# Kernel tuning notes

Hardware: AMD Instinct MI355X
Metric: run time of the kernel (lower is better)

Reference implementation:

```python
import jax, jax.numpy as jnp
import numpy as np

Nx, Nu, Ny, Np, H = 2, 1, 2, 8, 32
Nz = Np * (Nx + Nu)  # 24
B, T = 4096, 256
F, V, Delta = 0.1, 1.0, 1.0  # ps.squeeze(), volume, sample time
ymean = jnp.array([0.5, 0.5], jnp.float32)
ystd = jnp.array([0.3, 0.2], jnp.float32)
umean = jnp.array([1.0], jnp.float32)
ustd = jnp.array([0.5], jnp.float32)


def fnn(x, params):
    # dense layers: tanh hidden, linear output
    for W, b in params[:-1]:
        x = jnp.tanh(x @ W + b)
    W, b = params[-1]
    return x @ W + b


def fxzu(x, z, u, p1, p2, p3):
    # dCa/dt = F*(Caf-Ca)/V - r1 ; dCb/dt = -F*Cb/V + r1 - 3*r2 + r3
    Castd, Cbstd = ystd[0:1], ystd[1:2]
    r1 = fnn(x[:, 0:1], p1) * Castd
    r2 = fnn(x[:, 1:2], p2) * Cbstd
    r3 = fnn(z, p3) * Cbstd
    xs = x * ystd + ymean
    us = u * ustd + umean
    Ca, Cb, Caf = xs[:, 0:1], xs[:, 1:2], us[:, 0:1]
    dCa = F * (Caf - Ca) / V - r1
    dCb = -F * Cb / V + r1 - 3.0 * r2 + r3
    return jnp.concatenate([dCa, dCb], axis=-1) / ystd


def interp(yseq):
    # (B,(Np+1)*Nx) -> (B, Np*Nx): midpoints of consecutive Nx-blocks
    b = yseq.shape[0]
    y = yseq.reshape(b, Np + 1, Nx)
    return (0.5 * (y[:, :-1] + y[:, 1:])).reshape(b, Np * Nx)


def run(useq, xz0, p1, p2, p3):
    def step(xz, u):
        x, z = xz[:, :Nx], xz[:, Nx:]
        xpseq, upseq = z[:, :Np * Nx], z[:, Np * Nx:]
        k1 = fxzu(x, z, u, p1, p2, p3)
        z23 = jnp.concatenate([interp(jnp.concatenate([xpseq, x], -1)), upseq], -1)
        k2 = fxzu(x + Delta * k1 / 2, z23, u, p1, p2, p3)
        k3 = fxzu(x + Delta * k2 / 2, z23, u, p1, p2, p3)
        z4 = jnp.concatenate([xpseq[:, Nx:], x, upseq], -1)
        k4 = fxzu(x + Delta * k3, z4, u, p1, p2, p3)
        xplus = x + (Delta / 6.0) * (k1 + 2 * k2 + 2 * k3 + k4)
        zplus = jnp.concatenate([xpseq[:, Nx:], x, upseq[:, Nu:], u], -1)
        return jnp.concatenate([xplus, zplus], -1), x  # output is pre-update x
    _, ys = jax.lax.scan(step, xz0, jnp.swapaxes(useq, 0, 1))
    return jnp.swapaxes(ys, 0, 1)  # (B, T, Ny)


def setup_inputs() -> dict:
    key = jax.random.key(0)
    ks = jax.random.split(key, 12)
    inp = {
        'useq': jax.random.normal(ks[0], (B, T, Nu), jnp.float32),
        'xz0': jax.random.normal(ks[1], (B, Nx + Nz), jnp.float32),
    }
    dims = {'r1': [1, H, H, 1], 'r2': [1, H, H, 1], 'r3': [Nz, H, H, 1]}
    i = 2
    for name, ds in dims.items():
        for l, (din, dout) in enumerate(zip(ds[:-1], ds[1:])):
            inp[f'{name}W{l}'] = jax.random.normal(ks[i], (din, dout), jnp.float32) / np.sqrt(din).astype(np.float32)
            inp[f'{name}b{l}'] = jnp.zeros((dout,), jnp.float32)
            i += 1
    return inp


def reference(useq, xz0, r1W0, r1b0, r1W1, r1b1, r1W2, r1b2,
              r2W0, r2b0, r2W1, r2b1, r2W2, r2b2,
              r3W0, r3b0, r3W1, r3b1, r3W2, r3b2):
    p1 = [(r1W0, r1b0), (r1W1, r1b1), (r1W2, r1b2)]
    p2 = [(r2W0, r2b0), (r2W1, r2b1), (r2W2, r2b2)]
    p3 = [(r3W0, r3b0), (r3W1, r3b1), (r3W2, r3b2)]
    return run(useq, xz0, p1, p2, p3)
```

## Files before the change

kernel.cpp:

```cpp
#include <hip/hip_runtime.h>

#define DEVINL static __device__ __forceinline__
#define LDSBAR() asm volatile("s_waitcnt lgkmcnt(0)" ::: "memory")

DEVINL float tanh_fast(float x) {
  float e = __expf(2.0f * x);
  return 1.0f - 2.0f * __builtin_amdgcn_rcpf(e + 1.0f);
}

template <int CTRL>
DEVINL float dpp_add(float v) {
  int t = __builtin_amdgcn_update_dpp(0, __float_as_int(v), CTRL, 0xF, 0xF, true);
  return v + __int_as_float(t);
}
DEVINL float rsum32(float v) {
  v = dpp_add<0xB1>(v);
  v = dpp_add<0x4E>(v);
  v = dpp_add<0x141>(v);
  v = dpp_add<0x140>(v);
  v += __int_as_float(__builtin_amdgcn_ds_swizzle(__float_as_int(v), 0x401F));
  return v;
}

DEVINL float dot4(float4 v, const float* w) {
  return fmaf(v.x, w[0], fmaf(v.y, w[1], fmaf(v.z, w[2], v.w * w[3])));
}
DEVINL float dot32(const float4* hp, const float* W, float bias) {
  float a0 = bias, a1 = 0.f, a2 = 0.f, a3 = 0.f;
#pragma unroll
  for (int q = 0; q < 8; q += 4) {
    float4 h0 = hp[q], h1 = hp[q + 1], h2 = hp[q + 2], h3 = hp[q + 3];
    a0 = fmaf(h0.x, W[4 * q + 0], a0);  a0 = fmaf(h0.y, W[4 * q + 1], a0);
    a0 = fmaf(h0.z, W[4 * q + 2], a0);  a0 = fmaf(h0.w, W[4 * q + 3], a0);
    a1 = fmaf(h1.x, W[4 * q + 4], a1);  a1 = fmaf(h1.y, W[4 * q + 5], a1);
    a1 = fmaf(h1.z, W[4 * q + 6], a1);  a1 = fmaf(h1.w, W[4 * q + 7], a1);
    a2 = fmaf(h2.x, W[4 * q + 8], a2);  a2 = fmaf(h2.y, W[4 * q + 9], a2);
    a2 = fmaf(h2.z, W[4 * q + 10], a2); a2 = fmaf(h2.w, W[4 * q + 11], a2);
    a3 = fmaf(h3.x, W[4 * q + 12], a3); a3 = fmaf(h3.y, W[4 * q + 13], a3);
    a3 = fmaf(h3.z, W[4 * q + 14], a3); a3 = fmaf(h3.w, W[4 * q + 15], a3);
  }
  return (a0 + a1) + (a2 + a3);
}

constexpr int TSTEPS = 256;

__global__ __launch_bounds__(64, 2) void reac_kernel(
    const float* __restrict__ useq,
    const float* __restrict__ xz0,
    const float* __restrict__ r1W0, const float* __restrict__ r1b0,
    const float* __restrict__ r1W1, const float* __restrict__ r1b1,
    const float* __restrict__ r1W2, const float* __restrict__ r1b2,
    const float* __restrict__ r2W0, const float* __restrict__ r2b0,
    const float* __restrict__ r2W1, const float* __restrict__ r2b1,
    const float* __restrict__ r2W2, const float* __restrict__ r2b2,
    const float* __restrict__ r3W0, const float* __restrict__ r3b0,
    const float* __restrict__ r3W1, const float* __restrict__ r3b1,
    const float* __restrict__ r3W2, const float* __restrict__ r3b2,
    float2* __restrict__ out)
{
  const int lane = threadIdx.x;
  const int bl = lane >> 5;
  const int j  = lane & 31;
  const int b  = blockIdx.x * 2 + bl;

  float w0A = r1W0[j], b0A = r1b0[j];
  float w0B = r2W0[j], b0B = r2b0[j];
  float b1A = r1b1[j], b1B = r2b1[j];
  float w2A = r1W2[j], w2B = r2W2[j];
  float b2A = r1b2[0], b2B = r2b2[0];
  float b0C = r3b0[j], b1C = r3b1[j];
  float w2C = r3W2[j], b2C = r3b2[0];

  float W1A[32], W1B[32], W1C[32], W0C[24];
#pragma unroll
  for (int k = 0; k < 32; ++k) {
    W1A[k] = r1W1[k * 32 + j];
    W1B[k] = r2W1[k * 32 + j];
    W1C[k] = r3W1[k * 32 + j];
  }
#pragma unroll
  for (int k = 0; k < 24; ++k) W0C[k] = r3W0[k * 32 + j];

  __shared__ __align__(16) float zs[2][24];
  __shared__ __align__(16) float zb[2][16];
  __shared__ __align__(16) float hA[2][32];
  __shared__ __align__(16) float hB[2][32];
  __shared__ __align__(16) float hR3[2][3][32];

  float x0 = xz0[b * 26 + 0];
  float x1 = xz0[b * 26 + 1];
  if (j < 24) zs[bl][j] = xz0[b * 26 + 2 + j];
  LDSBAR();

  auto eval_r12 = [&](float s0, float s1, float& ra, float& rb) {
    float h1a = tanh_fast(fmaf(s0, w0A, b0A));
    float h1b = tanh_fast(fmaf(s1, w0B, b0B));
    hA[bl][j] = h1a;
    hB[bl][j] = h1b;
    LDSBAR();
    float aA = dot32((const float4*)&hA[bl][0], W1A, b1A);
    float aB = dot32((const float4*)&hB[bl][0], W1B, b1B);
    ra = (rsum32(tanh_fast(aA) * w2A) + b2A) * 0.3f;
    rb = (rsum32(tanh_fast(aB) * w2B) + b2B) * 0.2f;
  };

  auto mixk = [&](float sx0, float sx1, float Caf, float ra, float rb, float rc,
                  float& kx, float& ky) {
    float Ca = fmaf(sx0, 0.3f, 0.5f);
    float Cb = fmaf(sx1, 0.2f, 0.5f);
    float dCa = 0.1f * (Caf - Ca) - ra;
    float dCb = fmaf(-0.1f, Cb, ra - 3.0f * rb + rc);
    kx = dCa * (1.0f / 0.3f);
    ky = dCb * (1.0f / 0.2f);
  };

  float u = useq[b * TSTEPS];

  for (int t = 0; t < TSTEPS; ++t) {
    int tn = (t < TSTEPS - 1) ? (t + 1) : t;
    float u_nxt = useq[b * TSTEPS + tn];
    float Caf = fmaf(u, 0.5f, 1.0f);

    if (j == 0) out[b * TSTEPS + t] = make_float2(x0, x1);

    if (j < 16) {
      zb[bl][j] = (j < 14) ? zs[bl][j + 2] : ((j == 14) ? x0 : x1);
    }
    LDSBAR();

    const float4* zsp = (const float4*)&zs[bl][0];
    const float4* zbp = (const float4*)&zb[bl][0];
    float4 za0 = zsp[0], za1 = zsp[1], za2 = zsp[2], za3 = zsp[3];
    float4 zu0 = zsp[4], zu1 = zsp[5];
    float4 q0 = zbp[0], q1 = zbp[1], q2 = zbp[2], q3 = zbp[3];
    float accS = (dot4(za0, W0C) + dot4(za1, W0C + 4)) +
                 (dot4(za2, W0C + 8) + dot4(za3, W0C + 12));
    float accB = (dot4(q0, W0C) + dot4(q1, W0C + 4)) +
                 (dot4(q2, W0C + 8) + dot4(q3, W0C + 12));
    float accU = dot4(zu0, W0C + 16) + dot4(zu1, W0C + 20) + b0C;
    float a1v = accS + accU;
    float a4v = accB + accU;
    float a23v = fmaf(0.5f, accS + accB, accU);
    hR3[bl][0][j] = tanh_fast(a1v);
    hR3[bl][1][j] = tanh_fast(a23v);
    hR3[bl][2][j] = tanh_fast(a4v);
    LDSBAR();
    float o1 = dot32((const float4*)&hR3[bl][0][0], W1C, b1C);
    float o23 = dot32((const float4*)&hR3[bl][1][0], W1C, b1C);
    float o4 = dot32((const float4*)&hR3[bl][2][0], W1C, b1C);
    float rc1 = (rsum32(tanh_fast(o1) * w2C) + b2C) * 0.2f;
    float rc23 = (rsum32(tanh_fast(o23) * w2C) + b2C) * 0.2f;
    float rc4 = (rsum32(tanh_fast(o4) * w2C) + b2C) * 0.2f;

    float ra, rb, kx1, ky1, kx2, ky2, kx3, ky3, kx4, ky4;
    eval_r12(x0, x1, ra, rb);
    mixk(x0, x1, Caf, ra, rb, rc1, kx1, ky1);

    float sx = fmaf(kx1, 0.5f, x0), sy = fmaf(ky1, 0.5f, x1);
    eval_r12(sx, sy, ra, rb);
    mixk(sx, sy, Caf, ra, rb, rc23, kx2, ky2);

    sx = fmaf(kx2, 0.5f, x0); sy = fmaf(ky2, 0.5f, x1);
    eval_r12(sx, sy, ra, rb);
    mixk(sx, sy, Caf, ra, rb, rc23, kx3, ky3);

    sx = x0 + kx3; sy = x1 + ky3;
    eval_r12(sx, sy, ra, rb);
    mixk(sx, sy, Caf, ra, rb, rc4, kx4, ky4);

    float znew = 0.0f;
    if (j < 16) znew = zb[bl][j];
    else if (j < 23) znew = zs[bl][j + 1];
    else if (j == 23) znew = u;
    LDSBAR();
    if (j < 24) zs[bl][j] = znew;
    x0 += (kx1 + 2.0f * (kx2 + kx3) + kx4) * (1.0f / 6.0f);
    x1 += (ky1 + 2.0f * (ky2 + ky3) + ky4) * (1.0f / 6.0f);
    u = u_nxt;
    LDSBAR();
  }
}

extern "C" void kernel_launch(void* const* d_in, const int* in_sizes, int n_in,
                              void* d_out, int out_size, void* d_ws, size_t ws_size,
                              hipStream_t stream) {
  const float* p[20];
  for (int i = 0; i < 20; ++i) p[i] = (const float*)d_in[i];
  reac_kernel<<<dim3(2048), dim3(64), 0, stream>>>(
      p[0], p[1], p[2], p[3], p[4], p[5], p[6], p[7], p[8], p[9], p[10],
      p[11], p[12], p[13], p[14], p[15], p[16], p[17], p[18], p[19],
      (float2*)d_out);
}
```

Measured before the change: 943.9 us.

## Map one batch row per wavefront, splitting r1/r2 and r3 work across half-waves

```diff
diff --git a/kernel.cpp b/kernel.cpp
--- a/kernel.cpp
+++ b/kernel.cpp
@@ -25,26 +25,38 @@
 DEVINL float dot4(float4 v, const float* w) {
   return fmaf(v.x, w[0], fmaf(v.y, w[1], fmaf(v.z, w[2], v.w * w[3])));
 }
-DEVINL float dot32(const float4* hp, const float* W, float bias) {
+DEVINL float dot32(const float* hrow, const float* W, float bias) {
+  const float4* hp = (const float4*)hrow;
   float a0 = bias, a1 = 0.f, a2 = 0.f, a3 = 0.f;
 #pragma unroll
-  for (int q = 0; q < 8; q += 4) {
-    float4 h0 = hp[q], h1 = hp[q + 1], h2 = hp[q + 2], h3 = hp[q + 3];
-    a0 = fmaf(h0.x, W[4 * q + 0], a0);  a0 = fmaf(h0.y, W[4 * q + 1], a0);
-    a0 = fmaf(h0.z, W[4 * q + 2], a0);  a0 = fmaf(h0.w, W[4 * q + 3], a0);
-    a1 = fmaf(h1.x, W[4 * q + 4], a1);  a1 = fmaf(h1.y, W[4 * q + 5], a1);
-    a1 = fmaf(h1.z, W[4 * q + 6], a1);  a1 = fmaf(h1.w, W[4 * q + 7], a1);
-    a2 = fmaf(h2.x, W[4 * q + 8], a2);  a2 = fmaf(h2.y, W[4 * q + 9], a2);
-    a2 = fmaf(h2.z, W[4 * q + 10], a2); a2 = fmaf(h2.w, W[4 * q + 11], a2);
-    a3 = fmaf(h3.x, W[4 * q + 12], a3); a3 = fmaf(h3.y, W[4 * q + 13], a3);
-    a3 = fmaf(h3.z, W[4 * q + 14], a3); a3 = fmaf(h3.w, W[4 * q + 15], a3);
+  for (int q = 0; q < 8; q += 2) {
+    float4 x = hp[q], y = hp[q + 1];
+    a0 = fmaf(x.x, W[4 * q + 0], a0); a1 = fmaf(x.y, W[4 * q + 1], a1);
+    a2 = fmaf(x.z, W[4 * q + 2], a2); a3 = fmaf(x.w, W[4 * q + 3], a3);
+    a0 = fmaf(y.x, W[4 * q + 4], a0); a1 = fmaf(y.y, W[4 * q + 5], a1);
+    a2 = fmaf(y.z, W[4 * q + 6], a2); a3 = fmaf(y.w, W[4 * q + 7], a3);
   }
+  return (a0 + a1) + (a2 + a3);
+}
+DEVINL float pdot16(const float* hrow, const float* W) {
+  const float4* hp = (const float4*)hrow;
+  float a0 = 0.f, a1 = 0.f, a2 = 0.f, a3 = 0.f;
+  float4 x = hp[0], y = hp[1];
+  a0 = fmaf(x.x, W[0], a0);  a1 = fmaf(x.y, W[1], a1);
+  a2 = fmaf(x.z, W[2], a2);  a3 = fmaf(x.w, W[3], a3);
+  a0 = fmaf(y.x, W[4], a0);  a1 = fmaf(y.y, W[5], a1);
+  a2 = fmaf(y.z, W[6], a2);  a3 = fmaf(y.w, W[7], a3);
+  x = hp[2]; y = hp[3];
+  a0 = fmaf(x.x, W[8], a0);  a1 = fmaf(x.y, W[9], a1);
+  a2 = fmaf(x.z, W[10], a2); a3 = fmaf(x.w, W[11], a3);
+  a0 = fmaf(y.x, W[12], a0); a1 = fmaf(y.y, W[13], a1);
+  a2 = fmaf(y.z, W[14], a2); a3 = fmaf(y.w, W[15], a3);
   return (a0 + a1) + (a2 + a3);
 }
 
 constexpr int TSTEPS = 256;
 
-__global__ __launch_bounds__(64, 2) void reac_kernel(
+__global__ __launch_bounds__(64, 4) void reac_kernel(
     const float* __restrict__ useq,
     const float* __restrict__ xz0,
     const float* __restrict__ r1W0, const float* __restrict__ r1b0,
@@ -59,55 +71,56 @@
     float2* __restrict__ out)
 {
   const int lane = threadIdx.x;
-  const int bl = lane >> 5;
-  const int j  = lane & 31;
-  const int b  = blockIdx.x * 2 + bl;
+  const int j = lane & 31;
+  const bool hi = lane >= 32;
+  const int b = blockIdx.x;
 
-  float w0A = r1W0[j], b0A = r1b0[j];
-  float w0B = r2W0[j], b0B = r2b0[j];
-  float b1A = r1b1[j], b1B = r2b1[j];
-  float w2A = r1W2[j], w2B = r2W2[j];
-  float b2A = r1b2[0], b2B = r2b2[0];
-  float b0C = r3b0[j], b1C = r3b1[j];
-  float w2C = r3W2[j], b2C = r3b2[0];
+  const float* W0p = hi ? r2W0 : r1W0;
+  const float* B0p = hi ? r2b0 : r1b0;
+  const float* W1p = hi ? r2W1 : r1W1;
+  const float* B1p = hi ? r2b1 : r1b1;
+  const float* W2p = hi ? r2W2 : r1W2;
+  const float* B2p = hi ? r2b2 : r1b2;
+  float w0 = W0p[j], b0 = B0p[j], b1 = B1p[j], w2 = W2p[j], b2 = B2p[0];
+  float sc = hi ? 0.2f : 0.3f;
 
-  float W1A[32], W1B[32], W1C[32], W0C[24];
+  float W1[32];
 #pragma unroll
-  for (int k = 0; k < 32; ++k) {
-    W1A[k] = r1W1[k * 32 + j];
-    W1B[k] = r2W1[k * 32 + j];
-    W1C[k] = r3W1[k * 32 + j];
-  }
+  for (int k = 0; k < 32; ++k) W1[k] = W1p[k * 32 + j];
+
+  float W0C[24];
 #pragma unroll
-  for (int k = 0; k < 24; ++k) W0C[k] = r3W0[k * 32 + j];
+  for (int m = 0; m < 24; ++m) W0C[m] = r3W0[m * 32 + j];
+  const int kbase = hi ? 16 : 0;
+  float W1C[16];
+#pragma unroll
+  for (int k = 0; k < 16; ++k) W1C[k] = r3W1[(kbase + k) * 32 + j];
+  float b0C = r3b0[j], b1C = r3b1[j], w2C = r3W2[j], b2C = r3b2[0];
 
-  __shared__ __align__(16) float zs[2][24];
-  __shared__ __align__(16) float zb[2][16];
-  __shared__ __align__(16) float hA[2][32];
-  __shared__ __align__(16) float hB[2][32];
-  __shared__ __align__(16) float hR3[2][3][32];
+  __shared__ __align__(16) float zs[24];
+  __shared__ __align__(16) float zb[16];
+  __shared__ __align__(16) float h12[2][32];
+  __shared__ __align__(16) float hR3[3][32];
 
   float x0 = xz0[b * 26 + 0];
   float x1 = xz0[b * 26 + 1];
-  if (j < 24) zs[bl][j] = xz0[b * 26 + 2 + j];
+  if (!hi && j < 24) zs[j] = xz0[b * 26 + 2 + j];
   LDSBAR();
 
-  auto eval_r12 = [&](float s0, float s1, float& ra, float& rb) {
-    float h1a = tanh_fast(fmaf(s0, w0A, b0A));
-    float h1b = tanh_fast(fmaf(s1, w0B, b0B));
-    hA[bl][j] = h1a;
-    hB[bl][j] = h1b;
+  auto stage = [&](float sxv, float syv, float rc, float Caf,
+                   float& kx, float& ky) {
+    float s = hi ? syv : sxv;
+    float h = tanh_fast(fmaf(s, w0, b0));
     LDSBAR();
-    float aA = dot32((const float4*)&hA[bl][0], W1A, b1A);
-    float aB = dot32((const float4*)&hB[bl][0], W1B, b1B);
-    ra = (rsum32(tanh_fast(aA) * w2A) + b2A) * 0.3f;
-    rb = (rsum32(tanh_fast(aB) * w2B) + b2B) * 0.2f;
-  };
-
-  auto mixk = [&](float sx0, float sx1, float Caf, float ra, float rb, float rc,
-                  float& kx, float& ky) {
-    float Ca = fmaf(sx0, 0.3f, 0.5f);
-    float Cb = fmaf(sx1, 0.2f, 0.5f);
+    h12[hi][j] = h;
+    LDSBAR();
+    float a = dot32(&h12[hi][0], W1, b1);
+    float r = (rsum32(tanh_fast(a) * w2) + b2) * sc;
+    float rp = __shfl_xor(r, 32);
+    float ra = hi ? rp : r;
+    float rb = hi ? r : rp;
+    float Ca = fmaf(sxv, 0.3f, 0.5f);
+    float Cb = fmaf(syv, 0.2f, 0.5f);
     float dCa = 0.1f * (Caf - Ca) - ra;
     float dCb = fmaf(-0.1f, Cb, ra - 3.0f * rb + rc);
     kx = dCa * (1.0f / 0.3f);
@@ -121,59 +134,51 @@
     float u_nxt = useq[b * TSTEPS + tn];
     float Caf = fmaf(u, 0.5f, 1.0f);
 
-    if (j == 0) out[b * TSTEPS + t] = make_float2(x0, x1);
+    if (lane == 0) out[b * TSTEPS + t] = make_float2(x0, x1);
 
-    if (j < 16) {
-      zb[bl][j] = (j < 14) ? zs[bl][j + 2] : ((j == 14) ? x0 : x1);
+    if (!hi && j < 16) {
+      zb[j] = (j < 14) ? zs[j + 2] : ((j == 14) ? x0 : x1);
     }
     LDSBAR();
 
-    const float4* zsp = (const float4*)&zs[bl][0];
-    const float4* zbp = (const float4*)&zb[bl][0];
-    float4 za0 = zsp[0], za1 = zsp[1], za2 = zsp[2], za3 = zsp[3];
-    float4 zu0 = zsp[4], zu1 = zsp[5];
-    float4 q0 = zbp[0], q1 = zbp[1], q2 = zbp[2], q3 = zbp[3];
-    float accS = (dot4(za0, W0C) + dot4(za1, W0C + 4)) +
-                 (dot4(za2, W0C + 8) + dot4(za3, W0C + 12));
-    float accB = (dot4(q0, W0C) + dot4(q1, W0C + 4)) +
-                 (dot4(q2, W0C + 8) + dot4(q3, W0C + 12));
-    float accU = dot4(zu0, W0C + 16) + dot4(zu1, W0C + 20) + b0C;
-    float a1v = accS + accU;
-    float a4v = accB + accU;
-    float a23v = fmaf(0.5f, accS + accB, accU);
-    hR3[bl][0][j] = tanh_fast(a1v);
-    hR3[bl][1][j] = tanh_fast(a23v);
-    hR3[bl][2][j] = tanh_fast(a4v);
+    const float4* zp = (const float4*)(hi ? &zb[0] : &zs[0]);
+    float4 z0 = zp[0], z1 = zp[1], z2 = zp[2], z3 = zp[3];
+    const float4* up = (const float4*)&zs[16];
+    float4 u0 = up[0], u1 = up[1];
+    float A = b0C +
+        ((dot4(z0, W0C) + dot4(z1, W0C + 4)) +
+         (dot4(z2, W0C + 8) + dot4(z3, W0C + 12))) +
+        (dot4(u0, W0C + 16) + dot4(u1, W0C + 20));
+    float Ap = __shfl_xor(A, 32);
+    float tA = tanh_fast(A);
+    if (!hi) {
+      hR3[0][j] = tA;
+      hR3[1][j] = tanh_fast(0.5f * (A + Ap));
+    } else {
+      hR3[2][j] = tA;
+    }
     LDSBAR();
-    float o1 = dot32((const float4*)&hR3[bl][0][0], W1C, b1C);
-    float o23 = dot32((const float4*)&hR3[bl][1][0], W1C, b1C);
-    float o4 = dot32((const float4*)&hR3[bl][2][0], W1C, b1C);
-    float rc1 = (rsum32(tanh_fast(o1) * w2C) + b2C) * 0.2f;
-    float rc23 = (rsum32(tanh_fast(o23) * w2C) + b2C) * 0.2f;
-    float rc4 = (rsum32(tanh_fast(o4) * w2C) + b2C) * 0.2f;
+    float p0 = pdot16(&hR3[0][kbase], W1C);
+    float p1 = pdot16(&hR3[1][kbase], W1C);
+    float p2 = pdot16(&hR3[2][kbase], W1C);
+    float o0 = p0 + __shfl_xor(p0, 32) + b1C;
+    float o1 = p1 + __shfl_xor(p1, 32) + b1C;
+    float o2 = p2 + __shfl_xor(p2, 32) + b1C;
+    float rc1  = (rsum32(tanh_fast(o0) * w2C) + b2C) * 0.2f;
+    float rc23 = (rsum32(tanh_fast(o1) * w2C) + b2C) * 0.2f;
+    float rc4  = (rsum32(tanh_fast(o2) * w2C) + b2C) * 0.2f;
 
-    float ra, rb, kx1, ky1, kx2, ky2, kx3, ky3, kx4, ky4;
-    eval_r12(x0, x1, ra, rb);
-    mixk(x0, x1, Caf, ra, rb, rc1, kx1, ky1);
-
-    float sx = fmaf(kx1, 0.5f, x0), sy = fmaf(ky1, 0.5f, x1);
-    eval_r12(sx, sy, ra, rb);
-    mixk(sx, sy, Caf, ra, rb, rc23, kx2, ky2);
-
-    sx = fmaf(kx2, 0.5f, x0); sy = fmaf(ky2, 0.5f, x1);
-    eval_r12(sx, sy, ra, rb);
-    mixk(sx, sy, Caf, ra, rb, rc23, kx3, ky3);
-
-    sx = x0 + kx3; sy = x1 + ky3;
-    eval_r12(sx, sy, ra, rb);
-    mixk(sx, sy, Caf, ra, rb, rc4, kx4, ky4);
+    float kx1, ky1, kx2, ky2, kx3, ky3, kx4, ky4;
+    stage(x0, x1, rc1, Caf, kx1, ky1);
+    stage(fmaf(kx1, 0.5f, x0), fmaf(ky1, 0.5f, x1), rc23, Caf, kx2, ky2);
+    stage(fmaf(kx2, 0.5f, x0), fmaf(ky2, 0.5f, x1), rc23, Caf, kx3, ky3);
+    stage(x0 + kx3, x1 + ky3, rc4, Caf, kx4, ky4);
 
     float znew = 0.0f;
-    if (j < 16) znew = zb[bl][j];
-    else if (j < 23) znew = zs[bl][j + 1];
-    else if (j == 23) znew = u;
+    bool updz = (!hi) && (j < 24);
+    if (updz) znew = (j < 16) ? zb[j] : ((j < 23) ? zs[j + 1] : u);
     LDSBAR();
-    if (j < 24) zs[bl][j] = znew;
+    if (updz) zs[j] = znew;
     x0 += (kx1 + 2.0f * (kx2 + kx3) + kx4) * (1.0f / 6.0f);
     x1 += (ky1 + 2.0f * (ky2 + ky3) + ky4) * (1.0f / 6.0f);
     u = u_nxt;
@@ -186,7 +191,7 @@
                               hipStream_t stream) {
   const float* p[20];
   for (int i = 0; i < 20; ++i) p[i] = (const float*)d_in[i];
-  reac_kernel<<<dim3(2048), dim3(64), 0, stream>>>(
+  reac_kernel<<<dim3(4096), dim3(64), 0, stream>>>(
       p[0], p[1], p[2], p[3], p[4], p[5], p[6], p[7], p[8], p[9], p[10],
       p[11], p[12], p[13], p[14], p[15], p[16], p[17], p[18], p[19],
       (float2*)d_out);
```

Result: faster. 916.6 us (-2.9%).
